# Performance work log

Hardware: AMD Instinct MI355X
Metric: run time of the kernel (lower is better)

## Reference

```python
import jax, jax.numpy as jnp
import numpy as np

B, S, D, H, F = 2, 2048, 3072, 32, 8192
DH = D // H  # 96
EPS = 1e-5


def setup_inputs() -> dict:
    key = jax.random.key(0)
    ks = jax.random.split(key, 16)
    sd = 0.02
    inp = {
        "hidden_states": jax.random.normal(ks[0], (B, S, D), jnp.float32),
        "ln1_g": jnp.ones((D,), jnp.float32),
        "ln1_b": jnp.zeros((D,), jnp.float32),
        "Wq": jax.random.normal(ks[1], (D, H, DH), jnp.float32) * sd,
        "bq": jnp.zeros((H, DH), jnp.float32),
        "Wk": jax.random.normal(ks[2], (D, H, DH), jnp.float32) * sd,
        "bk": jnp.zeros((H, DH), jnp.float32),
        "Wv": jax.random.normal(ks[3], (D, H, DH), jnp.float32) * sd,
        "bv": jnp.zeros((H, DH), jnp.float32),
        "Wo": jax.random.normal(ks[4], (H, DH, D), jnp.float32) * sd,
        "bo": jnp.zeros((D,), jnp.float32),
        "ln2_g": jnp.ones((D,), jnp.float32),
        "ln2_b": jnp.zeros((D,), jnp.float32),
        "W1": jax.random.normal(ks[5], (D, F), jnp.float32) * sd,
        "b1": jnp.zeros((F,), jnp.float32),
        "W2": jax.random.normal(ks[6], (F, D), jnp.float32) * sd,
        "b2": jnp.zeros((D,), jnp.float32),
    }
    return inp


def _layernorm(x, g, b):
    m = jnp.mean(x, axis=-1, keepdims=True)
    v = jnp.mean(jnp.square(x - m), axis=-1, keepdims=True)
    return (x - m) * jax.lax.rsqrt(v + EPS) * g + b


def reference(hidden_states, ln1_g, ln1_b, Wq, bq, Wk, bk, Wv, bv, Wo, bo,
              ln2_g, ln2_b, W1, b1, W2, b2):
    # --- LN + self-attention + residual ---
    h = _layernorm(hidden_states, ln1_g, ln1_b)  # [B,S,D]
    q = jnp.einsum('bsd,dhk->bshk', h, Wq) + bq  # [B,S,H,DH]
    k = jnp.einsum('bsd,dhk->bshk', h, Wk) + bk
    v = jnp.einsum('bsd,dhk->bshk', h, Wv) + bv
    scale = 1.0 / np.sqrt(DH).astype(np.float32)
    scores = jnp.einsum('bshk,bthk->bhst', q, k) * scale  # [B,H,S,S]
    attn = jax.nn.softmax(scores, axis=-1)
    ctx = jnp.einsum('bhst,bthk->bshk', attn, v)  # [B,S,H,DH]
    attn_out = jnp.einsum('bshk,hkd->bsd', ctx, Wo) + bo
    h1 = hidden_states + attn_out
    # --- LN + MLP + residual ---
    h2 = _layernorm(h1, ln2_g, ln2_b)
    mlp = jax.nn.gelu(h2 @ W1 + b1, approximate=False) @ W2 + b2
    return h1 + mlp
```

## Files before the change

### kernel.cpp

```cpp
#include <hip/hip_runtime.h>
#include <math.h>

#define DEV __device__ __forceinline__

typedef __attribute__((ext_vector_type(8))) __bf16 bfrag;
typedef __attribute__((ext_vector_type(4))) float f4;
typedef __attribute__((ext_vector_type(8))) unsigned short u16x8;
typedef __attribute__((ext_vector_type(4))) unsigned short u16x4;

DEV unsigned short f2bf(float f) {
  unsigned u = __float_as_uint(f);
  u += 0x7fff + ((u >> 16) & 1);
  return (unsigned short)(u >> 16);
}

DEV void gload_lds16(const void* g, void* l) {
  __builtin_amdgcn_global_load_lds((const __attribute__((address_space(1))) void*)g,
                                   (__attribute__((address_space(3))) void*)l, 16, 0, 0);
}

template<int EPI, int OUTBF, int BIASROW>
__global__ __launch_bounds__(256, 2)
void gemm_bt(const unsigned short* __restrict__ A,
             const unsigned short* __restrict__ Bt,
             const float* __restrict__ bias,
             const float* __restrict__ res,
             void* __restrict__ outp,
             int M, int N, int K)
{
  __shared__ unsigned short As[2][128 * 32];
  __shared__ unsigned short Bs[2][128 * 32];
  const int tid = threadIdx.x;
  const int lane = tid & 63;
  const int wid = tid >> 6;
  const int wr = wid >> 1, wc = wid & 1;
  const int l15 = lane & 15, lg = lane >> 4;
  const long tM = (long)blockIdx.x * 128;
  const long tN = (long)blockIdx.y * 128;

  const int c0 = tid, c1 = tid + 256;
  const int r0 = c0 >> 2, k0 = (c0 & 3) * 8;
  const int r1 = c1 >> 2, k1 = (c1 & 3) * 8;

  const unsigned short* A0 = A + (tM + r0) * (long)K + k0;
  const unsigned short* A1 = A + (tM + r1) * (long)K + k1;
  const unsigned short* B0 = Bt + (tN + r0) * (long)K + k0;
  const unsigned short* B1 = Bt + (tN + r1) * (long)K + k1;

  auto stage = [&](int kt, int buf) {
    const long ko = (long)kt * 32;
    gload_lds16(A0 + ko, &As[buf][c0 * 8]);
    gload_lds16(A1 + ko, &As[buf][c1 * 8]);
    gload_lds16(B0 + ko, &Bs[buf][c0 * 8]);
    gload_lds16(B1 + ko, &Bs[buf][c1 * 8]);
  };

  stage(0, 0);
  f4 acc[4][4] = {};
  const int nk = K >> 5;
  int cur = 0;
  __syncthreads();
  for (int kt = 0; kt < nk; ++kt) {
    if (kt + 1 < nk) stage(kt + 1, cur ^ 1);
    bfrag aF[4], bF[4];
#pragma unroll
    for (int m = 0; m < 4; ++m)
      aF[m] = *(const bfrag*)&As[cur][(wr * 64 + m * 16 + l15) * 32 + lg * 8];
#pragma unroll
    for (int n = 0; n < 4; ++n)
      bF[n] = *(const bfrag*)&Bs[cur][(wc * 64 + n * 16 + l15) * 32 + lg * 8];
#pragma unroll
    for (int m = 0; m < 4; ++m)
#pragma unroll
      for (int n = 0; n < 4; ++n)
        acc[m][n] = __builtin_amdgcn_mfma_f32_16x16x32_bf16(aF[m], bF[n], acc[m][n], 0, 0, 0);
    __syncthreads();
    cur ^= 1;
  }

#pragma unroll
  for (int m = 0; m < 4; ++m) {
#pragma unroll
    for (int n = 0; n < 4; ++n) {
      const long col = tN + wc * 64 + n * 16 + l15;
      const float bcol = BIASROW ? 0.f : bias[col];
#pragma unroll
      for (int e = 0; e < 4; ++e) {
        const long row = tM + wr * 64 + m * 16 + lg * 4 + e;
        float v = acc[m][n][e] + (BIASROW ? bias[row] : bcol);
        if (EPI == 1) v = 0.5f * v * (1.0f + erff(v * 0.70710678118654752f));
        if (EPI == 2) v += res[row * N + col];
        if (OUTBF) ((unsigned short*)outp)[row * N + col] = f2bf(v);
        else       ((float*)outp)[row * N + col] = v;
      }
    }
  }
}

__global__ __launch_bounds__(256)
void ln_bf16(const float* __restrict__ x, const float* __restrict__ g,
             const float* __restrict__ b, unsigned short* __restrict__ out)
{
  __shared__ float red[4];
  const int tid = threadIdx.x;
  const long row = blockIdx.x;
  const float* xr = x + row * 3072;
  float4 v[3];
  float s = 0.f;
#pragma unroll
  for (int i = 0; i < 3; ++i) {
    v[i] = *(const float4*)&xr[i * 1024 + tid * 4];
    s += v[i].x + v[i].y + v[i].z + v[i].w;
  }
#pragma unroll
  for (int o = 32; o > 0; o >>= 1) s += __shfl_xor(s, o);
  if ((tid & 63) == 0) red[tid >> 6] = s;
  __syncthreads();
  s = red[0] + red[1] + red[2] + red[3];
  const float mean = s * (1.f / 3072.f);
  float vs = 0.f;
#pragma unroll
  for (int i = 0; i < 3; ++i) {
    const float dx = v[i].x - mean, dy = v[i].y - mean;
    const float dz = v[i].z - mean, dw = v[i].w - mean;
    vs += dx * dx + dy * dy + dz * dz + dw * dw;
  }
#pragma unroll
  for (int o = 32; o > 0; o >>= 1) vs += __shfl_xor(vs, o);
  __syncthreads();
  if ((tid & 63) == 0) red[tid >> 6] = vs;
  __syncthreads();
  vs = red[0] + red[1] + red[2] + red[3];
  const float rstd = rsqrtf(vs * (1.f / 3072.f) + 1e-5f);
#pragma unroll
  for (int i = 0; i < 3; ++i) {
    const int idx = i * 1024 + tid * 4;
    const float* vp = (const float*)&v[i];
    u16x4 o4;
#pragma unroll
    for (int c = 0; c < 4; ++c)
      o4[c] = f2bf((vp[c] - mean) * rstd * g[idx + c] + b[idx + c]);
    *(u16x4*)&out[row * 3072 + idx] = o4;
  }
}

__global__ __launch_bounds__(256)
void transpose_f32_bf16(const float* __restrict__ in, unsigned short* __restrict__ out,
                        int R, int C)
{
  __shared__ float tile[32][33];
  const int tx = threadIdx.x & 31, ty = threadIdx.x >> 5;
  const long r0 = (long)blockIdx.y * 32, cc0 = (long)blockIdx.x * 32;
#pragma unroll
  for (int i = 0; i < 4; ++i)
    tile[ty + 8 * i][tx] = in[(r0 + ty + 8 * i) * C + cc0 + tx];
  __syncthreads();
#pragma unroll
  for (int i = 0; i < 4; ++i)
    out[(cc0 + ty + 8 * i) * R + r0 + tx] = f2bf(tile[tx][ty + 8 * i]);
}

__global__ __launch_bounds__(256, 3)
void attn_fwd(const unsigned short* __restrict__ qg,
              const unsigned short* __restrict__ kg,
              const unsigned short* __restrict__ vT,
              unsigned short* __restrict__ ctx)
{
  __shared__ unsigned short Qs[64 * 104];
  __shared__ unsigned short Ks[64 * 104];
  __shared__ unsigned short Vt[96 * 72];
  __shared__ unsigned short Ps[4 * 16 * 72];
  const int tid = threadIdx.x;
  const int lane = tid & 63;
  const int w = tid >> 6;
  const int l15 = lane & 15, lg = lane >> 4;
  const int bid = (blockIdx.x & 7) * 256 + (blockIdx.x >> 3);
  const int qb = bid & 31;
  const int h = (bid >> 5) & 31;
  const int b = bid >> 10;
  const long base = ((long)b * 2048) * 3072 + h * 96;
  const long vbase = (long)(h * 96) * 4096 + (long)b * 2048;
  const int qbase = qb * 64;

#pragma unroll
  for (int i = 0; i < 3; ++i) {
    const int c = tid + i * 256;
    const int r = c / 12, c8 = (c % 12) * 8;
    *(u16x8*)&Qs[r * 104 + c8] = *(const u16x8*)&qg[base + (long)(qbase + r) * 3072 + c8];
  }

  float m_run = -1e30f, l_run = 0.f;
  f4 O[6] = {};
  const float sc = 0.1020620726f * 1.4426950409f;

  for (int t = 0; t < 32; ++t) {
    __syncthreads();
    const int kb = t * 64;
#pragma unroll
    for (int i = 0; i < 3; ++i) {
      const int c = tid + i * 256;
      const int r = c / 12, c8 = (c % 12) * 8;
      *(u16x8*)&Ks[r * 104 + c8] = *(const u16x8*)&kg[base + (long)(kb + r) * 3072 + c8];
    }
#pragma unroll
    for (int i = 0; i < 3; ++i) {
      const int idx = tid + i * 256;
      const int d = idx >> 3, c8 = (idx & 7) * 8;
      *(u16x8*)&Vt[d * 72 + c8] = *(const u16x8*)&vT[vbase + (long)d * 4096 + kb + c8];
    }
    __syncthreads();

    f4 sf[4];
#pragma unroll
    for (int mb = 0; mb < 4; ++mb) {
      f4 z = {0.f, 0.f, 0.f, 0.f};
      sf[mb] = z;
#pragma unroll
      for (int ks = 0; ks < 3; ++ks) {
        bfrag kf = *(const bfrag*)&Ks[(mb * 16 + l15) * 104 + ks * 32 + lg * 8];
        bfrag qf = *(const bfrag*)&Qs[(w * 16 + l15) * 104 + ks * 32 + lg * 8];
        sf[mb] = __builtin_amdgcn_mfma_f32_16x16x32_bf16(kf, qf, sf[mb], 0, 0, 0);
      }
    }
    float p[16];
    float tmax = -1e30f;
#pragma unroll
    for (int mb = 0; mb < 4; ++mb)
#pragma unroll
      for (int e = 0; e < 4; ++e) {
        const float sv = sf[mb][e] * sc;
        p[mb * 4 + e] = sv;
        tmax = fmaxf(tmax, sv);
      }
    tmax = fmaxf(tmax, __shfl_xor(tmax, 16));
    tmax = fmaxf(tmax, __shfl_xor(tmax, 32));
    const float mnew = fmaxf(m_run, tmax);
    const float alpha = exp2f(m_run - mnew);
    float psum = 0.f;
#pragma unroll
    for (int i = 0; i < 16; ++i) {
      p[i] = exp2f(p[i] - mnew);
      psum += p[i];
    }
    psum += __shfl_xor(psum, 16);
    psum += __shfl_xor(psum, 32);
    l_run = l_run * alpha + psum;
    m_run = mnew;
#pragma unroll
    for (int mb = 0; mb < 4; ++mb) {
      u16x4 pw;
#pragma unroll
      for (int e = 0; e < 4; ++e) pw[e] = f2bf(p[mb * 4 + e]);
      *(u16x4*)&Ps[w * 1152 + l15 * 72 + mb * 16 + lg * 4] = pw;
    }
    float aE[4];
#pragma unroll
    for (int e = 0; e < 4; ++e) aE[e] = __shfl(alpha, lg * 4 + e);
#pragma unroll
    for (int nb = 0; nb < 6; ++nb)
#pragma unroll
      for (int e = 0; e < 4; ++e) O[nb][e] *= aE[e];
#pragma unroll
    for (int nb = 0; nb < 6; ++nb)
#pragma unroll
      for (int ks = 0; ks < 2; ++ks) {
        bfrag pf = *(const bfrag*)&Ps[w * 1152 + l15 * 72 + ks * 32 + lg * 8];
        bfrag vf = *(const bfrag*)&Vt[(nb * 16 + l15) * 72 + ks * 32 + lg * 8];
        O[nb] = __builtin_amdgcn_mfma_f32_16x16x32_bf16(pf, vf, O[nb], 0, 0, 0);
      }
  }
  float lE[4];
#pragma unroll
  for (int e = 0; e < 4; ++e) lE[e] = 1.f / __shfl(l_run, lg * 4 + e);
#pragma unroll
  for (int nb = 0; nb < 6; ++nb)
#pragma unroll
    for (int e = 0; e < 4; ++e) {
      const long row = qbase + w * 16 + lg * 4 + e;
      ctx[base + row * 3072 + nb * 16 + l15] = f2bf(O[nb][e] * lE[e]);
    }
}

extern "C" void kernel_launch(void* const* d_in, const int* in_sizes, int n_in,
                              void* d_out, int out_size, void* d_ws, size_t ws_size,
                              hipStream_t stream)
{
  (void)in_sizes; (void)n_in; (void)out_size; (void)ws_size;
  const float* x    = (const float*)d_in[0];
  const float* ln1g = (const float*)d_in[1];
  const float* ln1b = (const float*)d_in[2];
  const float* Wq   = (const float*)d_in[3];
  const float* bq   = (const float*)d_in[4];
  const float* Wk   = (const float*)d_in[5];
  const float* bk   = (const float*)d_in[6];
  const float* Wv   = (const float*)d_in[7];
  const float* bv   = (const float*)d_in[8];
  const float* Wo   = (const float*)d_in[9];
  const float* bo   = (const float*)d_in[10];
  const float* ln2g = (const float*)d_in[11];
  const float* ln2b = (const float*)d_in[12];
  const float* W1   = (const float*)d_in[13];
  const float* b1   = (const float*)d_in[14];
  const float* W2   = (const float*)d_in[15];
  const float* b2   = (const float*)d_in[16];

  char* ws = (char*)d_ws;
  unsigned short* WqT = (unsigned short*)(ws + 0);
  unsigned short* WkT = (unsigned short*)(ws + 18874368);
  unsigned short* WvT = (unsigned short*)(ws + 37748736);
  unsigned short* WoT = (unsigned short*)(ws + 56623104);
  unsigned short* W1T = (unsigned short*)(ws + 75497472);
  unsigned short* W2T = (unsigned short*)(ws + 125829120);
  unsigned short* hbf  = (unsigned short*)(ws + 176160768);
  unsigned short* ctxb = hbf;
  unsigned short* qb_  = (unsigned short*)(ws + 201326592);
  unsigned short* h2   = qb_;
  unsigned short* kb_  = (unsigned short*)(ws + 226492416);
  unsigned short* act  = kb_;
  unsigned short* vb_  = (unsigned short*)(ws + 293601280);
  float*          h1   = (float*)(ws + 318767104);

  const dim3 blk(256);

  transpose_f32_bf16<<<dim3(96, 96),  blk, 0, stream>>>(Wq, WqT, 3072, 3072);
  transpose_f32_bf16<<<dim3(96, 96),  blk, 0, stream>>>(Wk, WkT, 3072, 3072);
  transpose_f32_bf16<<<dim3(96, 96),  blk, 0, stream>>>(Wv, WvT, 3072, 3072);
  transpose_f32_bf16<<<dim3(96, 96),  blk, 0, stream>>>(Wo, WoT, 3072, 3072);
  transpose_f32_bf16<<<dim3(256, 96), blk, 0, stream>>>(W1, W1T, 3072, 8192);
  transpose_f32_bf16<<<dim3(96, 256), blk, 0, stream>>>(W2, W2T, 8192, 3072);

  ln_bf16<<<4096, blk, 0, stream>>>(x, ln1g, ln1b, hbf);

  gemm_bt<0, 1, 0><<<dim3(32, 24), blk, 0, stream>>>(hbf, WqT, bq, nullptr, qb_, 4096, 3072, 3072);
  gemm_bt<0, 1, 0><<<dim3(32, 24), blk, 0, stream>>>(hbf, WkT, bk, nullptr, kb_, 4096, 3072, 3072);
  gemm_bt<0, 1, 1><<<dim3(24, 32), blk, 0, stream>>>(WvT, hbf, bv, nullptr, vb_, 3072, 4096, 3072);

  attn_fwd<<<2048, blk, 0, stream>>>(qb_, kb_, vb_, ctxb);

  gemm_bt<2, 0, 0><<<dim3(32, 24), blk, 0, stream>>>(ctxb, WoT, bo, x, h1, 4096, 3072, 3072);

  ln_bf16<<<4096, blk, 0, stream>>>(h1, ln2g, ln2b, h2);

  gemm_bt<1, 1, 0><<<dim3(32, 64), blk, 0, stream>>>(h2, W1T, b1, nullptr, act, 4096, 8192, 3072);
  gemm_bt<2, 0, 0><<<dim3(32, 24), blk, 0, stream>>>(act, W2T, b2, h1, (float*)d_out, 4096, 3072, 8192);
}
```

Measured before the change: 1.250 ms.

## Replace 128x128 GEMM with 256-row ping-pong tiled MFMA kernel, fuse Q/K projections

Replaces the 128x128, K=32 GEMM with a 512-thread kernel. It uses 256xBN tiles and K=64 stages, XOR-swizzled LDS, staged prefetch split across four compute phases with s_setprio, and a swizzled block-to-tile mapping. The Q and K projections are merged into one GEMM over concatenated weights and biases, and attention reads Q and K from the interleaved buffer. h1 is now stored directly in the output buffer. The larger tiles raise data reuse per LDS load but use far more LDS per block and depend on hand-tuned vmcnt waits.

```diff
diff --git a/kernel.cpp b/kernel.cpp
--- a/kernel.cpp
+++ b/kernel.cpp
@@ -19,79 +19,171 @@
                                    (__attribute__((address_space(3))) void*)l, 16, 0, 0);
 }
 
-template<int EPI, int OUTBF, int BIASROW>
-__global__ __launch_bounds__(256, 2)
-void gemm_bt(const unsigned short* __restrict__ A,
+template<int BN, int EPI, int OUTBF, int BIASROW>
+__global__ __launch_bounds__(512, 2)
+void gemm256(const unsigned short* __restrict__ A,
              const unsigned short* __restrict__ Bt,
              const float* __restrict__ bias,
              const float* __restrict__ res,
              void* __restrict__ outp,
-             int M, int N, int K)
+             int M, int N, int K, int gm)
 {
-  __shared__ unsigned short As[2][128 * 32];
-  __shared__ unsigned short Bs[2][128 * 32];
+  constexpr int NF  = BN / 64;
+  constexpr int NF2 = NF / 2;
+  constexpr int WTN = BN / 4;
+  __shared__ unsigned short As[2][256 * 64];
+  __shared__ unsigned short Bs[2][BN * 64];
+
   const int tid = threadIdx.x;
   const int lane = tid & 63;
   const int wid = tid >> 6;
-  const int wr = wid >> 1, wc = wid & 1;
+  const int wm = wid >> 2, wn = wid & 3;
   const int l15 = lane & 15, lg = lane >> 4;
-  const long tM = (long)blockIdx.x * 128;
-  const long tN = (long)blockIdx.y * 128;
-
-  const int c0 = tid, c1 = tid + 256;
-  const int r0 = c0 >> 2, k0 = (c0 & 3) * 8;
-  const int r1 = c1 >> 2, k1 = (c1 & 3) * 8;
-
-  const unsigned short* A0 = A + (tM + r0) * (long)K + k0;
-  const unsigned short* A1 = A + (tM + r1) * (long)K + k1;
-  const unsigned short* B0 = Bt + (tN + r0) * (long)K + k0;
-  const unsigned short* B1 = Bt + (tN + r1) * (long)K + k1;
-
-  auto stage = [&](int kt, int buf) {
-    const long ko = (long)kt * 32;
-    gload_lds16(A0 + ko, &As[buf][c0 * 8]);
-    gload_lds16(A1 + ko, &As[buf][c1 * 8]);
-    gload_lds16(B0 + ko, &Bs[buf][c0 * 8]);
-    gload_lds16(B1 + ko, &Bs[buf][c1 * 8]);
+
+  const int nwg = gridDim.x;
+  const int swz = (blockIdx.x & 7) * (nwg >> 3) + (blockIdx.x >> 3);
+  const int tm = swz % gm, tn = swz / gm;
+  const long tM = (long)tm * 256, tN = (long)tn * BN;
+
+  const int srow = tid >> 3;
+  const int lslot = (tid & 7) ^ (srow & 7);
+  const unsigned short* aSrc = A + (tM + srow) * (long)K + lslot * 8;
+  const unsigned short* bSrc = Bt + (tN + srow) * (long)K + lslot * 8;
+  const int NT = K >> 6;
+
+  auto stA = [&](int t, int j) {
+    gload_lds16(aSrc + (long)t * 64 + (long)j * 64 * K, &As[t & 1][j * 4096 + tid * 8]);
   };
-
-  stage(0, 0);
-  f4 acc[4][4] = {};
-  const int nk = K >> 5;
+  auto stB = [&](int t, int j) {
+    gload_lds16(bSrc + (long)t * 64 + (long)j * 64 * K, &Bs[t & 1][j * 4096 + tid * 8]);
+  };
+
+#pragma unroll
+  for (int j = 0; j < 4; ++j) stA(0, j);
+#pragma unroll
+  for (int j = 0; j < NF; ++j) stB(0, j);
+#pragma unroll
+  for (int j = 0; j < 4; ++j) stA(1, j);
+#pragma unroll
+  for (int j = 0; j < NF; ++j) stB(1, j);
+  if constexpr (BN == 256) asm volatile("s_waitcnt vmcnt(8)" ::: "memory");
+  else                     asm volatile("s_waitcnt vmcnt(6)" ::: "memory");
+  __builtin_amdgcn_s_barrier();
+
+  const int aRow = (wm * 128 + l15) * 64;
+  const int bRow = (wn * WTN + l15) * 64;
+  const int sx = l15 & 7;
+  const int sl0 = ((0 + lg) ^ sx) * 8;
+  const int sl1 = ((4 + lg) ^ sx) * 8;
+
+  bfrag aF[4][2], bF[NF][2];
+  f4 acc[8][NF] = {};
+
   int cur = 0;
-  __syncthreads();
-  for (int kt = 0; kt < nk; ++kt) {
-    if (kt + 1 < nk) stage(kt + 1, cur ^ 1);
-    bfrag aF[4], bF[4];
+  for (int t = 0; t < NT; ++t, cur ^= 1) {
+    const unsigned short* Ac = As[cur];
+    const unsigned short* Bc = Bs[cur];
+    const bool stg1 = (t >= 1) & (t + 1 < NT);
+    const bool stg2 = (t + 2 < NT);
+
+#pragma unroll
+    for (int m = 0; m < 4; ++m) {
+      aF[m][0] = *(const bfrag*)&Ac[aRow + m * 1024 + sl0];
+      aF[m][1] = *(const bfrag*)&Ac[aRow + m * 1024 + sl1];
+    }
+#pragma unroll
+    for (int n = 0; n < NF2; ++n) {
+      bF[n][0] = *(const bfrag*)&Bc[bRow + n * 1024 + sl0];
+      bF[n][1] = *(const bfrag*)&Bc[bRow + n * 1024 + sl1];
+    }
+    if (stg1) {
+      stA(t + 1, 1); stA(t + 1, 3);
+      if constexpr (BN == 256) { stB(t + 1, 2); stB(t + 1, 3); }
+      else                     { stB(t + 1, 0); stB(t + 1, 1); }
+    }
+    __builtin_amdgcn_s_barrier();
+    asm volatile("s_waitcnt lgkmcnt(0)" ::: "memory");
+    __builtin_amdgcn_sched_barrier(0);
+    __builtin_amdgcn_s_setprio(1);
 #pragma unroll
     for (int m = 0; m < 4; ++m)
-      aF[m] = *(const bfrag*)&As[cur][(wr * 64 + m * 16 + l15) * 32 + lg * 8];
-#pragma unroll
-    for (int n = 0; n < 4; ++n)
-      bF[n] = *(const bfrag*)&Bs[cur][(wc * 64 + n * 16 + l15) * 32 + lg * 8];
+#pragma unroll
+      for (int n = 0; n < NF2; ++n) {
+        acc[m][n] = __builtin_amdgcn_mfma_f32_16x16x32_bf16(aF[m][0], bF[n][0], acc[m][n], 0, 0, 0);
+        acc[m][n] = __builtin_amdgcn_mfma_f32_16x16x32_bf16(aF[m][1], bF[n][1], acc[m][n], 0, 0, 0);
+      }
+    __builtin_amdgcn_s_setprio(0);
+    __builtin_amdgcn_s_barrier();
+
+#pragma unroll
+    for (int n = NF2; n < NF; ++n) {
+      bF[n][0] = *(const bfrag*)&Bc[bRow + n * 1024 + sl0];
+      bF[n][1] = *(const bfrag*)&Bc[bRow + n * 1024 + sl1];
+    }
+    if constexpr (BN == 256) { if (stg1) { stB(t + 1, 0); stB(t + 1, 1); } }
+    __builtin_amdgcn_s_barrier();
+    asm volatile("s_waitcnt lgkmcnt(0)" ::: "memory");
+    __builtin_amdgcn_sched_barrier(0);
+    __builtin_amdgcn_s_setprio(1);
 #pragma unroll
     for (int m = 0; m < 4; ++m)
 #pragma unroll
-      for (int n = 0; n < 4; ++n)
-        acc[m][n] = __builtin_amdgcn_mfma_f32_16x16x32_bf16(aF[m], bF[n], acc[m][n], 0, 0, 0);
-    __syncthreads();
-    cur ^= 1;
-  }
-
-#pragma unroll
-  for (int m = 0; m < 4; ++m) {
-#pragma unroll
-    for (int n = 0; n < 4; ++n) {
-      const long col = tN + wc * 64 + n * 16 + l15;
-      const float bcol = BIASROW ? 0.f : bias[col];
+      for (int n = NF2; n < NF; ++n) {
+        acc[m][n] = __builtin_amdgcn_mfma_f32_16x16x32_bf16(aF[m][0], bF[n][0], acc[m][n], 0, 0, 0);
+        acc[m][n] = __builtin_amdgcn_mfma_f32_16x16x32_bf16(aF[m][1], bF[n][1], acc[m][n], 0, 0, 0);
+      }
+    __builtin_amdgcn_s_setprio(0);
+    __builtin_amdgcn_s_barrier();
+
+#pragma unroll
+    for (int m = 0; m < 4; ++m) {
+      aF[m][0] = *(const bfrag*)&Ac[aRow + 4096 + m * 1024 + sl0];
+      aF[m][1] = *(const bfrag*)&Ac[aRow + 4096 + m * 1024 + sl1];
+    }
+    if (stg2) { stA(t + 2, 0); stA(t + 2, 2); }
+    __builtin_amdgcn_s_barrier();
+    asm volatile("s_waitcnt lgkmcnt(0)" ::: "memory");
+    __builtin_amdgcn_sched_barrier(0);
+    __builtin_amdgcn_s_setprio(1);
+#pragma unroll
+    for (int m = 0; m < 4; ++m)
+#pragma unroll
+      for (int n = 0; n < NF2; ++n) {
+        acc[4 + m][n] = __builtin_amdgcn_mfma_f32_16x16x32_bf16(aF[m][0], bF[n][0], acc[4 + m][n], 0, 0, 0);
+        acc[4 + m][n] = __builtin_amdgcn_mfma_f32_16x16x32_bf16(aF[m][1], bF[n][1], acc[4 + m][n], 0, 0, 0);
+      }
+    __builtin_amdgcn_s_setprio(0);
+    __builtin_amdgcn_s_barrier();
+
+    __builtin_amdgcn_s_setprio(1);
+#pragma unroll
+    for (int m = 0; m < 4; ++m)
+#pragma unroll
+      for (int n = NF2; n < NF; ++n) {
+        acc[4 + m][n] = __builtin_amdgcn_mfma_f32_16x16x32_bf16(aF[m][0], bF[n][0], acc[4 + m][n], 0, 0, 0);
+        acc[4 + m][n] = __builtin_amdgcn_mfma_f32_16x16x32_bf16(aF[m][1], bF[n][1], acc[4 + m][n], 0, 0, 0);
+      }
+    __builtin_amdgcn_s_setprio(0);
+    if (t < NT - 2)       asm volatile("s_waitcnt vmcnt(2)" ::: "memory");
+    else if (t == NT - 2) asm volatile("s_waitcnt vmcnt(0)" ::: "memory");
+    __builtin_amdgcn_s_barrier();
+  }
+
+#pragma unroll
+  for (int m = 0; m < 8; ++m) {
+    const long row0 = tM + wm * 128 + m * 16 + lg * 4;
+#pragma unroll
+    for (int n = 0; n < NF; ++n) {
+      const long col = tN + wn * WTN + n * 16 + l15;
+      const float bc = BIASROW ? 0.f : bias[col];
 #pragma unroll
       for (int e = 0; e < 4; ++e) {
-        const long row = tM + wr * 64 + m * 16 + lg * 4 + e;
-        float v = acc[m][n][e] + (BIASROW ? bias[row] : bcol);
-        if (EPI == 1) v = 0.5f * v * (1.0f + erff(v * 0.70710678118654752f));
-        if (EPI == 2) v += res[row * N + col];
-        if (OUTBF) ((unsigned short*)outp)[row * N + col] = f2bf(v);
-        else       ((float*)outp)[row * N + col] = v;
+        const long row = row0 + e;
+        float v = acc[m][n][e] + (BIASROW ? bias[row] : bc);
+        if constexpr (EPI == 1) v = 0.5f * v * (1.0f + erff(v * 0.70710678118654752f));
+        if constexpr (EPI == 2) v += res[row * N + col];
+        if constexpr (OUTBF) ((unsigned short*)outp)[row * N + col] = f2bf(v);
+        else                 ((float*)outp)[row * N + col] = v;
       }
     }
   }
@@ -161,8 +253,7 @@
 }
 
 __global__ __launch_bounds__(256, 3)
-void attn_fwd(const unsigned short* __restrict__ qg,
-              const unsigned short* __restrict__ kg,
+void attn_fwd(const unsigned short* __restrict__ qk,
               const unsigned short* __restrict__ vT,
               unsigned short* __restrict__ ctx)
 {
@@ -178,15 +269,16 @@
   const int qb = bid & 31;
   const int h = (bid >> 5) & 31;
   const int b = bid >> 10;
-  const long base = ((long)b * 2048) * 3072 + h * 96;
-  const long vbase = (long)(h * 96) * 4096 + (long)b * 2048;
+  const long qkbase = ((long)b * 2048) * 6144 + h * 96;
+  const long obase  = ((long)b * 2048) * 3072 + h * 96;
+  const long vbase  = (long)(h * 96) * 4096 + (long)b * 2048;
   const int qbase = qb * 64;
 
 #pragma unroll
   for (int i = 0; i < 3; ++i) {
     const int c = tid + i * 256;
     const int r = c / 12, c8 = (c % 12) * 8;
-    *(u16x8*)&Qs[r * 104 + c8] = *(const u16x8*)&qg[base + (long)(qbase + r) * 3072 + c8];
+    *(u16x8*)&Qs[r * 104 + c8] = *(const u16x8*)&qk[qkbase + (long)(qbase + r) * 6144 + c8];
   }
 
   float m_run = -1e30f, l_run = 0.f;
@@ -200,7 +292,7 @@
     for (int i = 0; i < 3; ++i) {
       const int c = tid + i * 256;
       const int r = c / 12, c8 = (c % 12) * 8;
-      *(u16x8*)&Ks[r * 104 + c8] = *(const u16x8*)&kg[base + (long)(kb + r) * 3072 + c8];
+      *(u16x8*)&Ks[r * 104 + c8] = *(const u16x8*)&qk[qkbase + 3072 + (long)(kb + r) * 6144 + c8];
     }
 #pragma unroll
     for (int i = 0; i < 3; ++i) {
@@ -277,7 +369,7 @@
 #pragma unroll
     for (int e = 0; e < 4; ++e) {
       const long row = qbase + w * 16 + lg * 4 + e;
-      ctx[base + row * 3072 + nb * 16 + l15] = f2bf(O[nb][e] * lE[e]);
+      ctx[obase + row * 3072 + nb * 16 + l15] = f2bf(O[nb][e] * lE[e]);
     }
 }
 
@@ -305,42 +397,43 @@
   const float* b2   = (const float*)d_in[16];
 
   char* ws = (char*)d_ws;
-  unsigned short* WqT = (unsigned short*)(ws + 0);
-  unsigned short* WkT = (unsigned short*)(ws + 18874368);
-  unsigned short* WvT = (unsigned short*)(ws + 37748736);
-  unsigned short* WoT = (unsigned short*)(ws + 56623104);
-  unsigned short* W1T = (unsigned short*)(ws + 75497472);
-  unsigned short* W2T = (unsigned short*)(ws + 125829120);
-  unsigned short* hbf  = (unsigned short*)(ws + 176160768);
+  unsigned short* WqkT = (unsigned short*)(ws + 0);
+  unsigned short* WvT  = (unsigned short*)(ws + 37748736);
+  unsigned short* WoT  = (unsigned short*)(ws + 56623104);
+  unsigned short* W1T  = (unsigned short*)(ws + 75497472);
+  unsigned short* W2T  = (unsigned short*)(ws + 125829120);
+  float*          bqk  = (float*)(ws + 176160768);
+  unsigned short* hbf  = (unsigned short*)(ws + 176185344);
   unsigned short* ctxb = hbf;
-  unsigned short* qb_  = (unsigned short*)(ws + 201326592);
-  unsigned short* h2   = qb_;
-  unsigned short* kb_  = (unsigned short*)(ws + 226492416);
-  unsigned short* act  = kb_;
-  unsigned short* vb_  = (unsigned short*)(ws + 293601280);
-  float*          h1   = (float*)(ws + 318767104);
+  unsigned short* qkb  = (unsigned short*)(ws + 201351168);
+  unsigned short* h2   = qkb;
+  unsigned short* act  = (unsigned short*)(ws + 251682816);
+  unsigned short* vTb  = (unsigned short*)(ws + 318791680);
+  float*          h1   = (float*)d_out;
 
   const dim3 blk(256);
-
-  transpose_f32_bf16<<<dim3(96, 96),  blk, 0, stream>>>(Wq, WqT, 3072, 3072);
-  transpose_f32_bf16<<<dim3(96, 96),  blk, 0, stream>>>(Wk, WkT, 3072, 3072);
+  const dim3 blk512(512);
+
+  transpose_f32_bf16<<<dim3(96, 96),  blk, 0, stream>>>(Wq, WqkT, 3072, 3072);
+  transpose_f32_bf16<<<dim3(96, 96),  blk, 0, stream>>>(Wk, WqkT + 3072 * 3072, 3072, 3072);
   transpose_f32_bf16<<<dim3(96, 96),  blk, 0, stream>>>(Wv, WvT, 3072, 3072);
   transpose_f32_bf16<<<dim3(96, 96),  blk, 0, stream>>>(Wo, WoT, 3072, 3072);
   transpose_f32_bf16<<<dim3(256, 96), blk, 0, stream>>>(W1, W1T, 3072, 8192);
   transpose_f32_bf16<<<dim3(96, 256), blk, 0, stream>>>(W2, W2T, 8192, 3072);
+  hipMemcpyAsync(bqk, bq, 3072 * sizeof(float), hipMemcpyDeviceToDevice, stream);
+  hipMemcpyAsync(bqk + 3072, bk, 3072 * sizeof(float), hipMemcpyDeviceToDevice, stream);
 
   ln_bf16<<<4096, blk, 0, stream>>>(x, ln1g, ln1b, hbf);
 
-  gemm_bt<0, 1, 0><<<dim3(32, 24), blk, 0, stream>>>(hbf, WqT, bq, nullptr, qb_, 4096, 3072, 3072);
-  gemm_bt<0, 1, 0><<<dim3(32, 24), blk, 0, stream>>>(hbf, WkT, bk, nullptr, kb_, 4096, 3072, 3072);
-  gemm_bt<0, 1, 1><<<dim3(24, 32), blk, 0, stream>>>(WvT, hbf, bv, nullptr, vb_, 3072, 4096, 3072);
-
-  attn_fwd<<<2048, blk, 0, stream>>>(qb_, kb_, vb_, ctxb);
-
-  gemm_bt<2, 0, 0><<<dim3(32, 24), blk, 0, stream>>>(ctxb, WoT, bo, x, h1, 4096, 3072, 3072);
+  gemm256<256, 0, 1, 0><<<16 * 24, blk512, 0, stream>>>(hbf, WqkT, bqk, nullptr, qkb, 4096, 6144, 3072, 16);
+  gemm256<128, 0, 1, 1><<<12 * 32, blk512, 0, stream>>>(WvT, hbf, bv, nullptr, vTb, 3072, 4096, 3072, 12);
+
+  attn_fwd<<<2048, blk, 0, stream>>>(qkb, vTb, ctxb);
+
+  gemm256<128, 2, 0, 0><<<16 * 24, blk512, 0, stream>>>(ctxb, WoT, bo, x, h1, 4096, 3072, 3072, 16);
 
   ln_bf16<<<4096, blk, 0, stream>>>(h1, ln2g, ln2b, h2);
 
-  gemm_bt<1, 1, 0><<<dim3(32, 64), blk, 0, stream>>>(h2, W1T, b1, nullptr, act, 4096, 8192, 3072);
-  gemm_bt<2, 0, 0><<<dim3(32, 24), blk, 0, stream>>>(act, W2T, b2, h1, (float*)d_out, 4096, 3072, 8192);
-}
+  gemm256<256, 1, 1, 0><<<16 * 32, blk512, 0, stream>>>(h2, W1T, b1, nullptr, act, 4096, 8192, 3072, 16);
+  gemm256<128, 2, 0, 0><<<16 * 24, blk512, 0, stream>>>(act, W2T, b2, h1, (float*)d_out, 4096, 3072, 8192, 16);
+}
```

New measurement: 1.517 ms. 21.3% more time.

## Add XCD-aware GEMM tile swizzle and fuse Q/K projections into one GEMM

Applied to the files above, without the earlier changes.

The GEMM grid becomes 1D and is remapped so that blocks on the same XCD (blockIdx & 7) cover a contiguous group of M/N tiles. This is meant to improve per-XCD L2 reuse of the A and B panels. The Q and K weight transposes are packed into one [6144 x 3072] matrix with a concatenated bias, so a single GEMM produces interleaved Q/K. The attention kernel is changed to read that 6144-stride layout. h1 is now written directly into the output buffer, and the final GEMM adds the residual in place, which removes a workspace buffer but depends on each element being read before it is overwritten.

```diff
diff --git a/kernel.cpp b/kernel.cpp
--- a/kernel.cpp
+++ b/kernel.cpp
@@ -26,7 +26,7 @@
              const float* __restrict__ bias,
              const float* __restrict__ res,
              void* __restrict__ outp,
-             int M, int N, int K)
+             int M, int N, int K, int gm, int cm, int cn)
 {
   __shared__ unsigned short As[2][128 * 32];
   __shared__ unsigned short Bs[2][128 * 32];
@@ -35,8 +35,13 @@
   const int wid = tid >> 6;
   const int wr = wid >> 1, wc = wid & 1;
   const int l15 = lane & 15, lg = lane >> 4;
-  const long tM = (long)blockIdx.x * 128;
-  const long tN = (long)blockIdx.y * 128;
+
+  const int xcd = blockIdx.x & 7, bidx = blockIdx.x >> 3;
+  const int cgm = gm / cm;
+  const int tm = (xcd % cgm) * cm + bidx % cm;
+  const int tn = (xcd / cgm) * cn + bidx / cm;
+  const long tM = (long)tm * 128;
+  const long tN = (long)tn * 128;
 
   const int c0 = tid, c1 = tid + 256;
   const int r0 = c0 >> 2, k0 = (c0 & 3) * 8;
@@ -88,10 +93,10 @@
       for (int e = 0; e < 4; ++e) {
         const long row = tM + wr * 64 + m * 16 + lg * 4 + e;
         float v = acc[m][n][e] + (BIASROW ? bias[row] : bcol);
-        if (EPI == 1) v = 0.5f * v * (1.0f + erff(v * 0.70710678118654752f));
-        if (EPI == 2) v += res[row * N + col];
-        if (OUTBF) ((unsigned short*)outp)[row * N + col] = f2bf(v);
-        else       ((float*)outp)[row * N + col] = v;
+        if constexpr (EPI == 1) v = 0.5f * v * (1.0f + erff(v * 0.70710678118654752f));
+        if constexpr (EPI == 2) v += res[row * N + col];
+        if constexpr (OUTBF) ((unsigned short*)outp)[row * N + col] = f2bf(v);
+        else                 ((float*)outp)[row * N + col] = v;
       }
     }
   }
@@ -161,8 +166,7 @@
 }
 
 __global__ __launch_bounds__(256, 3)
-void attn_fwd(const unsigned short* __restrict__ qg,
-              const unsigned short* __restrict__ kg,
+void attn_fwd(const unsigned short* __restrict__ qk,
               const unsigned short* __restrict__ vT,
               unsigned short* __restrict__ ctx)
 {
@@ -178,15 +182,16 @@
   const int qb = bid & 31;
   const int h = (bid >> 5) & 31;
   const int b = bid >> 10;
-  const long base = ((long)b * 2048) * 3072 + h * 96;
-  const long vbase = (long)(h * 96) * 4096 + (long)b * 2048;
+  const long qkbase = ((long)b * 2048) * 6144 + h * 96;
+  const long obase  = ((long)b * 2048) * 3072 + h * 96;
+  const long vbase  = (long)(h * 96) * 4096 + (long)b * 2048;
   const int qbase = qb * 64;
 
 #pragma unroll
   for (int i = 0; i < 3; ++i) {
     const int c = tid + i * 256;
     const int r = c / 12, c8 = (c % 12) * 8;
-    *(u16x8*)&Qs[r * 104 + c8] = *(const u16x8*)&qg[base + (long)(qbase + r) * 3072 + c8];
+    *(u16x8*)&Qs[r * 104 + c8] = *(const u16x8*)&qk[qkbase + (long)(qbase + r) * 6144 + c8];
   }
 
   float m_run = -1e30f, l_run = 0.f;
@@ -200,7 +205,7 @@
     for (int i = 0; i < 3; ++i) {
       const int c = tid + i * 256;
       const int r = c / 12, c8 = (c % 12) * 8;
-      *(u16x8*)&Ks[r * 104 + c8] = *(const u16x8*)&kg[base + (long)(kb + r) * 3072 + c8];
+      *(u16x8*)&Ks[r * 104 + c8] = *(const u16x8*)&qk[qkbase + 3072 + (long)(kb + r) * 6144 + c8];
     }
 #pragma unroll
     for (int i = 0; i < 3; ++i) {
@@ -277,7 +282,7 @@
 #pragma unroll
     for (int e = 0; e < 4; ++e) {
       const long row = qbase + w * 16 + lg * 4 + e;
-      ctx[base + row * 3072 + nb * 16 + l15] = f2bf(O[nb][e] * lE[e]);
+      ctx[obase + row * 3072 + nb * 16 + l15] = f2bf(O[nb][e] * lE[e]);
     }
 }
 
@@ -305,42 +310,42 @@
   const float* b2   = (const float*)d_in[16];
 
   char* ws = (char*)d_ws;
-  unsigned short* WqT = (unsigned short*)(ws + 0);
-  unsigned short* WkT = (unsigned short*)(ws + 18874368);
-  unsigned short* WvT = (unsigned short*)(ws + 37748736);
-  unsigned short* WoT = (unsigned short*)(ws + 56623104);
-  unsigned short* W1T = (unsigned short*)(ws + 75497472);
-  unsigned short* W2T = (unsigned short*)(ws + 125829120);
-  unsigned short* hbf  = (unsigned short*)(ws + 176160768);
+  unsigned short* WqkT = (unsigned short*)(ws + 0);
+  unsigned short* WvT  = (unsigned short*)(ws + 37748736);
+  unsigned short* WoT  = (unsigned short*)(ws + 56623104);
+  unsigned short* W1T  = (unsigned short*)(ws + 75497472);
+  unsigned short* W2T  = (unsigned short*)(ws + 125829120);
+  float*          bqk  = (float*)(ws + 176160768);
+  unsigned short* hbf  = (unsigned short*)(ws + 176185344);
   unsigned short* ctxb = hbf;
-  unsigned short* qb_  = (unsigned short*)(ws + 201326592);
-  unsigned short* h2   = qb_;
-  unsigned short* kb_  = (unsigned short*)(ws + 226492416);
-  unsigned short* act  = kb_;
-  unsigned short* vb_  = (unsigned short*)(ws + 293601280);
-  float*          h1   = (float*)(ws + 318767104);
+  unsigned short* qkb  = (unsigned short*)(ws + 201351168);
+  unsigned short* h2   = qkb;
+  unsigned short* act  = (unsigned short*)(ws + 251682816);
+  unsigned short* vTb  = (unsigned short*)(ws + 318791680);
+  float*          h1   = (float*)d_out;
 
   const dim3 blk(256);
 
-  transpose_f32_bf16<<<dim3(96, 96),  blk, 0, stream>>>(Wq, WqT, 3072, 3072);
-  transpose_f32_bf16<<<dim3(96, 96),  blk, 0, stream>>>(Wk, WkT, 3072, 3072);
+  transpose_f32_bf16<<<dim3(96, 96),  blk, 0, stream>>>(Wq, WqkT, 3072, 3072);
+  transpose_f32_bf16<<<dim3(96, 96),  blk, 0, stream>>>(Wk, WqkT + 3072 * 3072, 3072, 3072);
   transpose_f32_bf16<<<dim3(96, 96),  blk, 0, stream>>>(Wv, WvT, 3072, 3072);
   transpose_f32_bf16<<<dim3(96, 96),  blk, 0, stream>>>(Wo, WoT, 3072, 3072);
   transpose_f32_bf16<<<dim3(256, 96), blk, 0, stream>>>(W1, W1T, 3072, 8192);
   transpose_f32_bf16<<<dim3(96, 256), blk, 0, stream>>>(W2, W2T, 8192, 3072);
+  hipMemcpyAsync(bqk, bq, 3072 * sizeof(float), hipMemcpyDeviceToDevice, stream);
+  hipMemcpyAsync(bqk + 3072, bk, 3072 * sizeof(float), hipMemcpyDeviceToDevice, stream);
 
   ln_bf16<<<4096, blk, 0, stream>>>(x, ln1g, ln1b, hbf);
 
-  gemm_bt<0, 1, 0><<<dim3(32, 24), blk, 0, stream>>>(hbf, WqT, bq, nullptr, qb_, 4096, 3072, 3072);
-  gemm_bt<0, 1, 0><<<dim3(32, 24), blk, 0, stream>>>(hbf, WkT, bk, nullptr, kb_, 4096, 3072, 3072);
-  gemm_bt<0, 1, 1><<<dim3(24, 32), blk, 0, stream>>>(WvT, hbf, bv, nullptr, vb_, 3072, 4096, 3072);
-
-  attn_fwd<<<2048, blk, 0, stream>>>(qb_, kb_, vb_, ctxb);
-
-  gemm_bt<2, 0, 0><<<dim3(32, 24), blk, 0, stream>>>(ctxb, WoT, bo, x, h1, 4096, 3072, 3072);
+  gemm_bt<0, 1, 0><<<1536, blk, 0, stream>>>(hbf, WqkT, bqk, nullptr, qkb, 4096, 6144, 3072, 32, 16, 12);
+  gemm_bt<0, 1, 1><<<768, blk, 0, stream>>>(WvT, hbf, bv, nullptr, vTb, 3072, 4096, 3072, 24, 12, 8);
+
+  attn_fwd<<<2048, blk, 0, stream>>>(qkb, vTb, ctxb);
+
+  gemm_bt<2, 0, 0><<<768, blk, 0, stream>>>(ctxb, WoT, bo, x, h1, 4096, 3072, 3072, 32, 16, 6);
 
   ln_bf16<<<4096, blk, 0, stream>>>(h1, ln2g, ln2b, h2);
 
-  gemm_bt<1, 1, 0><<<dim3(32, 64), blk, 0, stream>>>(h2, W1T, b1, nullptr, act, 4096, 8192, 3072);
-  gemm_bt<2, 0, 0><<<dim3(32, 24), blk, 0, stream>>>(act, W2T, b2, h1, (float*)d_out, 4096, 3072, 8192);
-}
+  gemm_bt<1, 1, 0><<<2048, blk, 0, stream>>>(h2, W1T, b1, nullptr, act, 4096, 8192, 3072, 32, 16, 16);
+  gemm_bt<2, 0, 0><<<768, blk, 0, stream>>>(act, W2T, b2, h1, (float*)d_out, 4096, 3072, 8192, 32, 16, 6);
+}
```

After: 1.269 ms. Within noise of the previous version (+1.5%).
